# Kernel tuning notes

Measured on AMD Instinct MI355X. Metric: run time of the kernel, lower is better.

The kernel has to match this reference:

```python
import jax, jax.numpy as jnp
import numpy as np

N, D = 8192, 1024


def setup_inputs() -> dict:
    key = jax.random.key(0)
    k1, k2, k3, k4 = jax.random.split(key, 4)
    return {
        "first_features": jax.random.normal(k1, (N, D), dtype=jnp.float32),
        "second_features": jax.random.normal(k2, (N, D), dtype=jnp.float32),
        "first_label": jax.random.randint(k3, (N,), 0, N, dtype=jnp.int64),
        "second_label": jax.random.randint(k4, (N,), 0, N, dtype=jnp.int64),
        "logit_scale": jnp.asarray(10.0, dtype=jnp.float32),
        "logit_bias": jnp.asarray(-10.0, dtype=jnp.float32),
    }


def reference(first_features, second_features, first_label, second_label,
              logit_scale, logit_bias):
    # logits: [N, N] = scale * A @ B^T + bias
    logits = logit_scale * jnp.einsum("id,jd->ij", first_features, second_features)
    logits = logits + logit_bias
    # ground truth: +1 where labels match, -1 elsewhere
    labels = jnp.where(first_label[:, None] == second_label[None, :], 1.0, -1.0)
    labels = labels.astype(logits.dtype)
    # loss = sum(-logsigmoid(labels * logits)) / N  (mask_diagonal=False)
    loss = -jnp.sum(jax.nn.log_sigmoid(labels * logits)) / first_features.shape[0]
    return loss
```

## Files before the change

### kernel.cpp

```cpp
#include <hip/hip_runtime.h>
#include <hip/hip_bf16.h>
#include <stdint.h>

#define N_TOK 8192
#define D_K   1024
#define NB    128
#define NT    16
#define GSTRIDE 32768

typedef __attribute__((ext_vector_type(4)))  int   i32x4;
typedef __attribute__((ext_vector_type(8)))  int   i32x8;
typedef __attribute__((ext_vector_type(16))) float f32x16;

__global__ void zero_out_kernel(float* out) { out[0] = 0.0f; }

__device__ __forceinline__ unsigned int f32_to_e4m3(float x) {
  uint32_t u = __builtin_bit_cast(uint32_t, x);
  unsigned int s = (u >> 24) & 0x80u;
  float ax = __builtin_fabsf(x);
  if (ax < 0.015625f) {
    int q = (int)rintf(ax * 512.0f);
    return s | (unsigned int)q;
  }
  uint32_t au = u & 0x7FFFFFFFu;
  uint32_t v = au + 0x7FFFFu + ((au >> 20) & 1u);
  int em = (int)(v >> 20) - 960;
  if (em > 0x7E) em = 0x7E;
  return s | (unsigned int)em;
}

__global__ void __launch_bounds__(256)
convert_perm_kernel(const float* __restrict__ a, const float* __restrict__ b,
                    unsigned char* __restrict__ oa,
                    unsigned char* __restrict__ ob) {
  __shared__ unsigned int P[8192];
  const int blk = (int)blockIdx.x;
  const int g   = blk >> 1;
  const float* __restrict__ src = (blk & 1) ? b : a;
  unsigned char* __restrict__ dst = (blk & 1) ? ob : oa;
  const int tid = threadIdx.x;

  const float4* s4 = (const float4*)src + (size_t)g * 8192;
  const int koff = (tid >> 4) * 512 + ((tid >> 3) & 1) * 256 + (tid & 7);
#pragma unroll
  for (int i = 0; i < 32; ++i) {
    float4 v = s4[i * 256 + tid];
    unsigned int w = f32_to_e4m3(v.x) | (f32_to_e4m3(v.y) << 8) |
                     (f32_to_e4m3(v.z) << 16) | (f32_to_e4m3(v.w) << 24);
    P[koff + i * 8] = w;
  }
  __syncthreads();
  i32x4* d4 = (i32x4*)(dst + (size_t)g * GSTRIDE);
  const i32x4* p4 = (const i32x4*)P;
#pragma unroll
  for (int i = 0; i < 8; ++i) d4[i * 256 + tid] = p4[i * 256 + tid];
}

__global__ void __launch_bounds__(256)
sigc_kernel(const unsigned char* __restrict__ A8,
            const unsigned char* __restrict__ B8,
            const int* __restrict__ labA, const int* __restrict__ labB,
            const float* __restrict__ scale_p, const float* __restrict__ bias_p,
            float* __restrict__ out) {
  __shared__ int sLabA[NB];
  __shared__ int sLabB[NB];
  __shared__ float sPart[4];

  const int tid  = threadIdx.x;
  const int lane = tid & 63;
  const int wid  = tid >> 6;
  const int wr   = wid >> 1;
  const int wc   = wid & 1;

  const int bid = (int)blockIdx.x;
  const int xcd = bid & 7;
  const int ii  = bid >> 3;
  const int rr  = (xcd >> 1) * 16 + (ii & 15);
  const int cc  = (xcd & 1) * 32 + (ii >> 4);

  if (tid < 128)      sLabA[tid] = labA[rr * NB + tid];
  else                sLabB[tid - 128] = labB[cc * NB + (tid - 128)];

  const unsigned char* aF[2];
  const unsigned char* bF[2];
#pragma unroll
  for (int f = 0; f < 2; ++f) {
    aF[f] = A8 + (size_t)(rr * 4 + wr * 2 + f) * GSTRIDE + lane * 32;
    bF[f] = B8 + (size_t)(cc * 4 + wc * 2 + f) * GSTRIDE + lane * 32;
  }

#define LOADT(fa, fb, T) do {                                              \
    fa[0] = *(const i32x8*)(aF[0] + (T) * 2048);                           \
    fa[1] = *(const i32x8*)(aF[1] + (T) * 2048);                           \
    fb[0] = *(const i32x8*)(bF[0] + (T) * 2048);                           \
    fb[1] = *(const i32x8*)(bF[1] + (T) * 2048);                           \
  } while (0)

#define MMAT(fa, fb) do {                                                  \
    __builtin_amdgcn_s_setprio(1);                                         \
    acc00 = __builtin_amdgcn_mfma_scale_f32_32x32x64_f8f6f4(               \
        fa[0], fb[0], acc00, 0, 0, 0, 0x7F7F7F7F, 0, 0x7F7F7F7F);          \
    acc01 = __builtin_amdgcn_mfma_scale_f32_32x32x64_f8f6f4(               \
        fa[0], fb[1], acc01, 0, 0, 0, 0x7F7F7F7F, 0, 0x7F7F7F7F);          \
    acc10 = __builtin_amdgcn_mfma_scale_f32_32x32x64_f8f6f4(               \
        fa[1], fb[0], acc10, 0, 0, 0, 0x7F7F7F7F, 0, 0x7F7F7F7F);          \
    acc11 = __builtin_amdgcn_mfma_scale_f32_32x32x64_f8f6f4(               \
        fa[1], fb[1], acc11, 0, 0, 0, 0x7F7F7F7F, 0, 0x7F7F7F7F);          \
    __builtin_amdgcn_s_setprio(0); } while (0)

  f32x16 acc00 = {0}, acc01 = {0}, acc10 = {0}, acc11 = {0};

  i32x8 fA0[2], fB0[2], fA1[2], fB1[2];

  LOADT(fA0, fB0, 0);

#pragma unroll
  for (int t2 = 0; t2 < NT / 2; ++t2) {
    const int e = 2 * t2;
    LOADT(fA1, fB1, e + 1);
    MMAT(fA0, fB0);
    if (t2 < NT / 2 - 1) LOADT(fA0, fB0, e + 2);
    MMAT(fA1, fB1);
  }

  __syncthreads();

  const float L2E = 1.4426950408889634f;
  const float sl2e = scale_p[0] * L2E;
  const float bl2e = bias_p[0] * L2E;
  const int colIn = lane & 31;
  const int hi32  = lane >> 5;
  const int colL0 = sLabB[wc * 64 + colIn];
  const int colL1 = sLabB[wc * 64 + 32 + colIn];
  int rl0[16], rl1[16];
#pragma unroll
  for (int r = 0; r < 16; ++r) {
    const int rbase = (r & 3) + 8 * (r >> 2) + 4 * hi32;
    rl0[r] = sLabA[wr * 64 + rbase];
    rl1[r] = sLabA[wr * 64 + 32 + rbase];
  }

  float S1 = 0.f, S2 = 0.f, Sm = 0.f, p = 1.0f;
#define EPI(ACC, RL, CL) do {                                              \
    _Pragma("unroll") for (int _r = 0; _r < 16; ++_r) {                    \
      const float _u = fmaf(sl2e, ACC[_r], bl2e);                          \
      S1 += _u;                                                            \
      S2 += fabsf(_u);                                                     \
      const float _e = exp2f(-fabsf(_u));                                  \
      p = fmaf(p, _e, p);                                                  \
      if (RL[_r] == (CL)) Sm += _u;                                       \
    } } while (0)

  EPI(acc00, rl0, colL0);
  EPI(acc01, rl0, colL1);
  EPI(acc10, rl1, colL0);
  EPI(acc11, rl1, colL1);

  float loss = 0.5f * (S1 + S2) - Sm + log2f(p);

#pragma unroll
  for (int off = 32; off > 0; off >>= 1) loss += __shfl_down(loss, off, 64);
  if (lane == 0) sPart[wid] = loss;
  __syncthreads();
  if (tid == 0) {
    const float s = (sPart[0] + sPart[1]) + (sPart[2] + sPart[3]);
    atomicAdd(out, s * (0.6931471805599453f / (float)N_TOK));
  }
}

extern "C" void kernel_launch(void* const* d_in, const int* in_sizes, int n_in,
                              void* d_out, int out_size, void* d_ws, size_t ws_size,
                              hipStream_t stream) {
  const float* a  = (const float*)d_in[0];
  const float* b  = (const float*)d_in[1];
  const int*   la = (const int*)d_in[2];
  const int*   lb = (const int*)d_in[3];
  const float* sc = (const float*)d_in[4];
  const float* bi = (const float*)d_in[5];
  float* out = (float*)d_out;

  unsigned char* wa = (unsigned char*)d_ws;
  unsigned char* wb = wa + (size_t)N_TOK * D_K;

  zero_out_kernel<<<1, 1, 0, stream>>>(out);
  convert_perm_kernel<<<512, 256, 0, stream>>>(a, b, wa, wb);
  const int grid = (N_TOK / NB) * (N_TOK / NB);
  sigc_kernel<<<grid, 256, 0, stream>>>(wa, wb, la, lb, sc, bi, out);
}
```

Before: 105.6 us.

## Fold output zeroing into convert kernel, simplify MFMA loop, split epilogue accumulators

Drops the separate single-thread zeroing kernel by having block 0 of the convert kernel clear the output, which removes one kernel launch. The manual two-stage register double-buffering in the fp8 MFMA loop becomes a plain unrolled loop, leaving load and MFMA scheduling to the compiler. The epilogue now keeps four independent sets of partial sums and products to shorten dependency chains. It also swaps exp2f/log2f for the raw amdgcn exp2 and log intrinsics and makes the label-match add branchless. The risks are weaker load/compute overlap in the main loop and slightly different rounding from the hardware transcendental instructions.

```diff
diff --git a/kernel.cpp b/kernel.cpp
--- a/kernel.cpp
+++ b/kernel.cpp
@@ -11,8 +11,6 @@
 typedef __attribute__((ext_vector_type(4)))  int   i32x4;
 typedef __attribute__((ext_vector_type(8)))  int   i32x8;
 typedef __attribute__((ext_vector_type(16))) float f32x16;
-
-__global__ void zero_out_kernel(float* out) { out[0] = 0.0f; }
 
 __device__ __forceinline__ unsigned int f32_to_e4m3(float x) {
   uint32_t u = __builtin_bit_cast(uint32_t, x);
@@ -32,9 +30,11 @@
 __global__ void __launch_bounds__(256)
 convert_perm_kernel(const float* __restrict__ a, const float* __restrict__ b,
                     unsigned char* __restrict__ oa,
-                    unsigned char* __restrict__ ob) {
+                    unsigned char* __restrict__ ob,
+                    float* __restrict__ out) {
   __shared__ unsigned int P[8192];
   const int blk = (int)blockIdx.x;
+  if (blk == 0 && threadIdx.x == 0) out[0] = 0.0f;
   const int g   = blk >> 1;
   const float* __restrict__ src = (blk & 1) ? b : a;
   unsigned char* __restrict__ dst = (blk & 1) ? ob : oa;
@@ -81,46 +81,29 @@
   if (tid < 128)      sLabA[tid] = labA[rr * NB + tid];
   else                sLabB[tid - 128] = labB[cc * NB + (tid - 128)];
 
-  const unsigned char* aF[2];
-  const unsigned char* bF[2];
-#pragma unroll
-  for (int f = 0; f < 2; ++f) {
-    aF[f] = A8 + (size_t)(rr * 4 + wr * 2 + f) * GSTRIDE + lane * 32;
-    bF[f] = B8 + (size_t)(cc * 4 + wc * 2 + f) * GSTRIDE + lane * 32;
-  }
-
-#define LOADT(fa, fb, T) do {                                              \
-    fa[0] = *(const i32x8*)(aF[0] + (T) * 2048);                           \
-    fa[1] = *(const i32x8*)(aF[1] + (T) * 2048);                           \
-    fb[0] = *(const i32x8*)(bF[0] + (T) * 2048);                           \
-    fb[1] = *(const i32x8*)(bF[1] + (T) * 2048);                           \
-  } while (0)
-
-#define MMAT(fa, fb) do {                                                  \
-    __builtin_amdgcn_s_setprio(1);                                         \
-    acc00 = __builtin_amdgcn_mfma_scale_f32_32x32x64_f8f6f4(               \
-        fa[0], fb[0], acc00, 0, 0, 0, 0x7F7F7F7F, 0, 0x7F7F7F7F);          \
-    acc01 = __builtin_amdgcn_mfma_scale_f32_32x32x64_f8f6f4(               \
-        fa[0], fb[1], acc01, 0, 0, 0, 0x7F7F7F7F, 0, 0x7F7F7F7F);          \
-    acc10 = __builtin_amdgcn_mfma_scale_f32_32x32x64_f8f6f4(               \
-        fa[1], fb[0], acc10, 0, 0, 0, 0x7F7F7F7F, 0, 0x7F7F7F7F);          \
-    acc11 = __builtin_amdgcn_mfma_scale_f32_32x32x64_f8f6f4(               \
-        fa[1], fb[1], acc11, 0, 0, 0, 0x7F7F7F7F, 0, 0x7F7F7F7F);          \
-    __builtin_amdgcn_s_setprio(0); } while (0)
+  const unsigned char* aF0 = A8 + (size_t)(rr * 4 + wr * 2) * GSTRIDE + lane * 32;
+  const unsigned char* aF1 = aF0 + GSTRIDE;
+  const unsigned char* bF0 = B8 + (size_t)(cc * 4 + wc * 2) * GSTRIDE + lane * 32;
+  const unsigned char* bF1 = bF0 + GSTRIDE;
 
   f32x16 acc00 = {0}, acc01 = {0}, acc10 = {0}, acc11 = {0};
 
-  i32x8 fA0[2], fB0[2], fA1[2], fB1[2];
-
-  LOADT(fA0, fB0, 0);
-
 #pragma unroll
-  for (int t2 = 0; t2 < NT / 2; ++t2) {
-    const int e = 2 * t2;
-    LOADT(fA1, fB1, e + 1);
-    MMAT(fA0, fB0);
-    if (t2 < NT / 2 - 1) LOADT(fA0, fB0, e + 2);
-    MMAT(fA1, fB1);
+  for (int t = 0; t < NT; ++t) {
+    i32x8 fa0 = *(const i32x8*)(aF0 + t * 2048);
+    i32x8 fa1 = *(const i32x8*)(aF1 + t * 2048);
+    i32x8 fb0 = *(const i32x8*)(bF0 + t * 2048);
+    i32x8 fb1 = *(const i32x8*)(bF1 + t * 2048);
+    __builtin_amdgcn_s_setprio(1);
+    acc00 = __builtin_amdgcn_mfma_scale_f32_32x32x64_f8f6f4(
+        fa0, fb0, acc00, 0, 0, 0, 0x7F7F7F7F, 0, 0x7F7F7F7F);
+    acc01 = __builtin_amdgcn_mfma_scale_f32_32x32x64_f8f6f4(
+        fa0, fb1, acc01, 0, 0, 0, 0x7F7F7F7F, 0, 0x7F7F7F7F);
+    acc10 = __builtin_amdgcn_mfma_scale_f32_32x32x64_f8f6f4(
+        fa1, fb0, acc10, 0, 0, 0, 0x7F7F7F7F, 0, 0x7F7F7F7F);
+    acc11 = __builtin_amdgcn_mfma_scale_f32_32x32x64_f8f6f4(
+        fa1, fb1, acc11, 0, 0, 0, 0x7F7F7F7F, 0, 0x7F7F7F7F);
+    __builtin_amdgcn_s_setprio(0);
   }
 
   __syncthreads();
@@ -140,23 +123,31 @@
     rl1[r] = sLabA[wr * 64 + 32 + rbase];
   }
 
-  float S1 = 0.f, S2 = 0.f, Sm = 0.f, p = 1.0f;
-#define EPI(ACC, RL, CL) do {                                              \
+  float S1a = 0.f, S2a = 0.f, Sma = 0.f, pa = 1.0f;
+  float S1b = 0.f, S2b = 0.f, Smb = 0.f, pb = 1.0f;
+  float S1c = 0.f, S2c = 0.f, Smc = 0.f, pc = 1.0f;
+  float S1d = 0.f, S2d = 0.f, Smd = 0.f, pd = 1.0f;
+
+#define EPI(ACC, RL, CL, S1x, S2x, Smx, px) do {                           \
     _Pragma("unroll") for (int _r = 0; _r < 16; ++_r) {                    \
       const float _u = fmaf(sl2e, ACC[_r], bl2e);                          \
-      S1 += _u;                                                            \
-      S2 += fabsf(_u);                                                     \
-      const float _e = exp2f(-fabsf(_u));                                  \
-      p = fmaf(p, _e, p);                                                  \
-      if (RL[_r] == (CL)) Sm += _u;                                       \
+      const float _au = fabsf(_u);                                         \
+      S1x += _u;                                                           \
+      S2x += _au;                                                          \
+      px = fmaf(px, __builtin_amdgcn_exp2f(-_au), px);                     \
+      Smx += (RL[_r] == (CL)) ? _u : 0.0f;                                 \
     } } while (0)
 
-  EPI(acc00, rl0, colL0);
-  EPI(acc01, rl0, colL1);
-  EPI(acc10, rl1, colL0);
-  EPI(acc11, rl1, colL1);
+  EPI(acc00, rl0, colL0, S1a, S2a, Sma, pa);
+  EPI(acc01, rl0, colL1, S1b, S2b, Smb, pb);
+  EPI(acc10, rl1, colL0, S1c, S2c, Smc, pc);
+  EPI(acc11, rl1, colL1, S1d, S2d, Smd, pd);
 
-  float loss = 0.5f * (S1 + S2) - Sm + log2f(p);
+  const float S1 = (S1a + S1b) + (S1c + S1d);
+  const float S2 = (S2a + S2b) + (S2c + S2d);
+  const float Sm = (Sma + Smb) + (Smc + Smd);
+  const float pp = (pa * pb) * (pc * pd);
+  float loss = 0.5f * (S1 + S2) - Sm + __builtin_amdgcn_logf(pp);
 
 #pragma unroll
   for (int off = 32; off > 0; off >>= 1) loss += __shfl_down(loss, off, 64);
@@ -182,8 +173,7 @@
   unsigned char* wa = (unsigned char*)d_ws;
   unsigned char* wb = wa + (size_t)N_TOK * D_K;
 
-  zero_out_kernel<<<1, 1, 0, stream>>>(out);
-  convert_perm_kernel<<<512, 256, 0, stream>>>(a, b, wa, wb);
+  convert_perm_kernel<<<512, 256, 0, stream>>>(a, b, wa, wb, out);
   const int grid = (N_TOK / NB) * (N_TOK / NB);
   sigc_kernel<<<grid, 256, 0, stream>>>(wa, wb, la, lb, sc, bi, out);
 }
```

Result: slower. 161.5 us (+52.9%).
